# Kernel tuning notes

Hardware: AMD Instinct MI355X
Metric: run time of the kernel (lower is better)

Reference implementation:

```python
import jax, jax.numpy as jnp
import numpy as np

PED = 1024
R_DIM = 128
M_DIM = 128


def setup_inputs() -> dict:
    key = jax.random.key(0)
    k1, k2, k3, k4, k5 = jax.random.split(key, 5)
    hidden_state = jax.random.normal(k1, (PED, M_DIM), dtype=jnp.float32)
    rela_state = jax.random.normal(k2, (PED, PED, R_DIM), dtype=jnp.float32)
    corr_index = jax.random.normal(k3, (PED, PED, 2), dtype=jnp.float32)
    nei_index = jax.random.randint(k4, (PED, PED), 0, 2, dtype=jnp.int32)
    att_w = jax.random.normal(k5, (R_DIM,), dtype=jnp.float32) * 0.2  # nn.Linear weight, std=0.2 init
    att_b = jnp.zeros((1,), dtype=jnp.float32)
    return {"hidden_state": hidden_state, "rela_state": rela_state,
            "corr_index": corr_index, "nei_index": nei_index,
            "att_w": att_w, "att_b": att_b}


def reference(hidden_state, rela_state, corr_index, nei_index, att_w, att_b):
    # hidden_state: [P, M], rela_state: [P, P, R], nei_index: [P, P]
    P = hidden_state.shape[0]
    mask = nei_index.reshape(P, P) > 0                      # [P, P]
    # Linear attention score per (i, j) relation feature
    scores = jnp.einsum('ijr,r->ij', rela_state.reshape(P, P, -1), att_w) + att_b[0]
    # Non-neighbor slots stay 0 then are replaced by -1e-6 (original: Pos[Pos==0] = -1e-6)
    pos = jnp.where(mask, scores, jnp.float32(-1e-6))
    pos = jax.nn.softmax(pos, axis=1)                       # softmax over neighbors j
    # H[i, j] = hidden_state[j] * pos[i, j] where masked, else 0; then sum over j
    weights = jnp.where(mask, pos, 0.0)                     # [P, P]
    H_sum = jnp.einsum('ij,jm->im', weights, hidden_state)  # [P, M]
    return H_sum
```

## Files before the change

kernel.cpp:

```cpp
#include <hip/hip_runtime.h>
#include <math.h>

#define P_DIM 1024
#define R_DIM 128
#define M_DIM 128

__global__ __launch_bounds__(256) void scores_kernel(
    const float* __restrict__ rela,
    const float* __restrict__ att_w,
    const float* __restrict__ att_b,
    float* __restrict__ scores)
{
    const int t    = blockIdx.x * 256 + threadIdx.x;
    const int pair = t >> 5;
    const int lane = t & 31;

    const float4 w4 = reinterpret_cast<const float4*>(att_w)[lane];
    const float4 v  = reinterpret_cast<const float4*>(rela)[(size_t)pair * 32 + lane];

    float s = v.x * w4.x + v.y * w4.y + v.z * w4.z + v.w * w4.w;
    s += __shfl_xor(s, 16);
    s += __shfl_xor(s, 8);
    s += __shfl_xor(s, 4);
    s += __shfl_xor(s, 2);
    s += __shfl_xor(s, 1);

    if (lane == 0) scores[pair] = s + att_b[0];
}

__device__ __forceinline__ float fcomp(const float4& v, int k) {
    return k == 0 ? v.x : k == 1 ? v.y : k == 2 ? v.z : v.w;
}

__global__ __launch_bounds__(256) void attn_kernel(
    const float* __restrict__ scores,
    const int* __restrict__ nei,
    const float* __restrict__ hidden,
    float* __restrict__ out)
{
    __shared__ float  wsm[4][P_DIM];
    __shared__ float4 part[4][8][32];

    const int t    = threadIdx.x;
    const int wid  = t >> 6;
    const int lane = t & 63;
    const int i0   = blockIdx.x << 2;
    const int i    = i0 + wid;

    const float4* s4p = reinterpret_cast<const float4*>(scores + (size_t)i * P_DIM);
    const int4*   n4p = reinterpret_cast<const int4*>(nei + (size_t)i * P_DIM);

    float pv[16];
    unsigned mbits = 0;
    float lmax = -3.0e38f;
    #pragma unroll
    for (int c = 0; c < 4; ++c) {
        const int idx = c * 64 + lane;
        const float4 s4 = s4p[idx];
        const int4   n4 = n4p[idx];
        const float v0 = (n4.x > 0) ? s4.x : -1e-6f;
        const float v1 = (n4.y > 0) ? s4.y : -1e-6f;
        const float v2 = (n4.z > 0) ? s4.z : -1e-6f;
        const float v3 = (n4.w > 0) ? s4.w : -1e-6f;
        mbits |= ((n4.x > 0) ? 1u : 0u) << (c * 4 + 0);
        mbits |= ((n4.y > 0) ? 1u : 0u) << (c * 4 + 1);
        mbits |= ((n4.z > 0) ? 1u : 0u) << (c * 4 + 2);
        mbits |= ((n4.w > 0) ? 1u : 0u) << (c * 4 + 3);
        pv[c * 4 + 0] = v0; pv[c * 4 + 1] = v1;
        pv[c * 4 + 2] = v2; pv[c * 4 + 3] = v3;
        lmax = fmaxf(lmax, fmaxf(fmaxf(v0, v1), fmaxf(v2, v3)));
    }
    #pragma unroll
    for (int off = 32; off >= 1; off >>= 1)
        lmax = fmaxf(lmax, __shfl_xor(lmax, off));

    float lsum = 0.f;
    #pragma unroll
    for (int k = 0; k < 16; ++k) {
        const float e = __expf(pv[k] - lmax);
        pv[k] = e;
        lsum += e;
    }
    #pragma unroll
    for (int off = 32; off >= 1; off >>= 1)
        lsum += __shfl_xor(lsum, off);
    const float inv = 1.0f / lsum;

    #pragma unroll
    for (int c = 0; c < 4; ++c) {
        const int idx = c * 64 + lane;
        float4 o;
        o.x = ((mbits >> (c * 4 + 0)) & 1u) ? pv[c * 4 + 0] * inv : 0.f;
        o.y = ((mbits >> (c * 4 + 1)) & 1u) ? pv[c * 4 + 1] * inv : 0.f;
        o.z = ((mbits >> (c * 4 + 2)) & 1u) ? pv[c * 4 + 2] * inv : 0.f;
        o.w = ((mbits >> (c * 4 + 3)) & 1u) ? pv[c * 4 + 3] * inv : 0.f;
        reinterpret_cast<float4*>(wsm[wid])[idx] = o;
    }
    __syncthreads();

    const int c4 = t & 31;
    const int h  = t >> 5;

    float4 acc[4];
    #pragma unroll
    for (int r = 0; r < 4; ++r) acc[r] = make_float4(0.f, 0.f, 0.f, 0.f);

    const int jbase = h * 128;
    #pragma unroll 2
    for (int jq = 0; jq < 32; ++jq) {
        const int j = jbase + jq * 4;
        float4 wq[4];
        #pragma unroll
        for (int r = 0; r < 4; ++r)
            wq[r] = *reinterpret_cast<const float4*>(&wsm[r][j]);
        float4 hv[4];
        #pragma unroll
        for (int k = 0; k < 4; ++k)
            hv[k] = reinterpret_cast<const float4*>(hidden + (size_t)(j + k) * M_DIM)[c4];
        #pragma unroll
        for (int r = 0; r < 4; ++r) {
            #pragma unroll
            for (int k = 0; k < 4; ++k) {
                const float wc = fcomp(wq[r], k);
                acc[r].x += wc * hv[k].x;
                acc[r].y += wc * hv[k].y;
                acc[r].z += wc * hv[k].z;
                acc[r].w += wc * hv[k].w;
            }
        }
    }

    #pragma unroll
    for (int r = 0; r < 4; ++r) part[r][h][c4] = acc[r];
    __syncthreads();

    if (t < 128) {
        const int r = t >> 5;
        const int c = t & 31;
        float4 sum = part[r][0][c];
        #pragma unroll
        for (int hh = 1; hh < 8; ++hh) {
            const float4 p = part[r][hh][c];
            sum.x += p.x; sum.y += p.y; sum.z += p.z; sum.w += p.w;
        }
        reinterpret_cast<float4*>(out + (size_t)(i0 + r) * M_DIM)[c] = sum;
    }
}

extern "C" void kernel_launch(void* const* d_in, const int* in_sizes, int n_in,
                              void* d_out, int out_size, void* d_ws, size_t ws_size,
                              hipStream_t stream) {
    const float* hidden = (const float*)d_in[0];
    const float* rela   = (const float*)d_in[1];
    const int*   nei    = (const int*)d_in[3];
    const float* att_w  = (const float*)d_in[4];
    const float* att_b  = (const float*)d_in[5];
    float* out    = (float*)d_out;
    float* scores = (float*)d_ws;

    scores_kernel<<<(P_DIM * P_DIM) / 8, 256, 0, stream>>>(rela, att_w, att_b, scores);
    attn_kernel<<<P_DIM / 4, 256, 0, stream>>>(scores, nei, hidden, out);
}
```

Measured before the change: 685.3 us.

## Fuse score computation, softmax and weighted sum into one per-row kernel

Replaces the two-kernel pipeline with a single kernel where each block handles one row i: it computes the relation scores into shared memory, does a block-wide masked softmax, then accumulates the weighted sum of hidden rows. This removes the scores round-trip through global memory and one launch. In exchange the grid shrinks to one block per row, reducing memory-level parallelism on the large rela stream. Each block also rereads all of hidden instead of sharing it across four rows.

```diff
diff --git a/kernel.cpp b/kernel.cpp
--- a/kernel.cpp
+++ b/kernel.cpp
@@ -5,145 +5,104 @@
 #define R_DIM 128
 #define M_DIM 128
 
-__global__ __launch_bounds__(256) void scores_kernel(
+__global__ __launch_bounds__(256) void fused_kernel(
     const float* __restrict__ rela,
+    const int*   __restrict__ nei,
+    const float* __restrict__ hidden,
     const float* __restrict__ att_w,
     const float* __restrict__ att_b,
-    float* __restrict__ scores)
-{
-    const int t    = blockIdx.x * 256 + threadIdx.x;
-    const int pair = t >> 5;
-    const int lane = t & 31;
-
-    const float4 w4 = reinterpret_cast<const float4*>(att_w)[lane];
-    const float4 v  = reinterpret_cast<const float4*>(rela)[(size_t)pair * 32 + lane];
-
-    float s = v.x * w4.x + v.y * w4.y + v.z * w4.z + v.w * w4.w;
-    s += __shfl_xor(s, 16);
-    s += __shfl_xor(s, 8);
-    s += __shfl_xor(s, 4);
-    s += __shfl_xor(s, 2);
-    s += __shfl_xor(s, 1);
-
-    if (lane == 0) scores[pair] = s + att_b[0];
-}
-
-__device__ __forceinline__ float fcomp(const float4& v, int k) {
-    return k == 0 ? v.x : k == 1 ? v.y : k == 2 ? v.z : v.w;
-}
-
-__global__ __launch_bounds__(256) void attn_kernel(
-    const float* __restrict__ scores,
-    const int* __restrict__ nei,
-    const float* __restrict__ hidden,
     float* __restrict__ out)
 {
-    __shared__ float  wsm[4][P_DIM];
-    __shared__ float4 part[4][8][32];
+    __shared__ float  s_lds[P_DIM];
+    __shared__ float  red[8];
+    __shared__ float2 part[4][64];
 
-    const int t    = threadIdx.x;
-    const int wid  = t >> 6;
-    const int lane = t & 63;
-    const int i0   = blockIdx.x << 2;
-    const int i    = i0 + wid;
+    const int t   = threadIdx.x;
+    const int i   = blockIdx.x;
+    const int g   = t >> 5;
+    const int l32 = t & 31;
 
-    const float4* s4p = reinterpret_cast<const float4*>(scores + (size_t)i * P_DIM);
-    const int4*   n4p = reinterpret_cast<const int4*>(nei + (size_t)i * P_DIM);
+    const float4 w4 = reinterpret_cast<const float4*>(att_w)[l32];
+    const float4* rrow =
+        reinterpret_cast<const float4*>(rela + (size_t)i * (P_DIM * R_DIM));
 
-    float pv[16];
-    unsigned mbits = 0;
-    float lmax = -3.0e38f;
-    #pragma unroll
-    for (int c = 0; c < 4; ++c) {
-        const int idx = c * 64 + lane;
-        const float4 s4 = s4p[idx];
-        const int4   n4 = n4p[idx];
-        const float v0 = (n4.x > 0) ? s4.x : -1e-6f;
-        const float v1 = (n4.y > 0) ? s4.y : -1e-6f;
-        const float v2 = (n4.z > 0) ? s4.z : -1e-6f;
-        const float v3 = (n4.w > 0) ? s4.w : -1e-6f;
-        mbits |= ((n4.x > 0) ? 1u : 0u) << (c * 4 + 0);
-        mbits |= ((n4.y > 0) ? 1u : 0u) << (c * 4 + 1);
-        mbits |= ((n4.z > 0) ? 1u : 0u) << (c * 4 + 2);
-        mbits |= ((n4.w > 0) ? 1u : 0u) << (c * 4 + 3);
-        pv[c * 4 + 0] = v0; pv[c * 4 + 1] = v1;
-        pv[c * 4 + 2] = v2; pv[c * 4 + 3] = v3;
-        lmax = fmaxf(lmax, fmaxf(fmaxf(v0, v1), fmaxf(v2, v3)));
+    #pragma unroll 4
+    for (int jq = 0; jq < 128; ++jq) {
+        const int j = jq * 8 + g;
+        const float4 v = rrow[(size_t)j * 32 + l32];
+        float s = v.x * w4.x + v.y * w4.y + v.z * w4.z + v.w * w4.w;
+        s += __shfl_xor(s, 16);
+        s += __shfl_xor(s, 8);
+        s += __shfl_xor(s, 4);
+        s += __shfl_xor(s, 2);
+        s += __shfl_xor(s, 1);
+        if (l32 == 0) s_lds[j] = s;
     }
+    __syncthreads();
+
+    const float bias = att_b[0];
+    const int4  n4 = reinterpret_cast<const int4*>(nei + (size_t)i * P_DIM)[t];
+    const float4 sv = reinterpret_cast<const float4*>(s_lds)[t];
+
+    float v0 = (n4.x > 0) ? sv.x + bias : -1e-6f;
+    float v1 = (n4.y > 0) ? sv.y + bias : -1e-6f;
+    float v2 = (n4.z > 0) ? sv.z + bias : -1e-6f;
+    float v3 = (n4.w > 0) ? sv.w + bias : -1e-6f;
+
+    float lmax = fmaxf(fmaxf(v0, v1), fmaxf(v2, v3));
     #pragma unroll
     for (int off = 32; off >= 1; off >>= 1)
         lmax = fmaxf(lmax, __shfl_xor(lmax, off));
+    if ((t & 63) == 0) red[t >> 6] = lmax;
+    __syncthreads();
+    const float gmax = fmaxf(fmaxf(red[0], red[1]), fmaxf(red[2], red[3]));
 
-    float lsum = 0.f;
-    #pragma unroll
-    for (int k = 0; k < 16; ++k) {
-        const float e = __expf(pv[k] - lmax);
-        pv[k] = e;
-        lsum += e;
-    }
+    const float e0 = __expf(v0 - gmax);
+    const float e1 = __expf(v1 - gmax);
+    const float e2 = __expf(v2 - gmax);
+    const float e3 = __expf(v3 - gmax);
+    float lsum = (e0 + e1) + (e2 + e3);
     #pragma unroll
     for (int off = 32; off >= 1; off >>= 1)
         lsum += __shfl_xor(lsum, off);
-    const float inv = 1.0f / lsum;
+    if ((t & 63) == 0) red[4 + (t >> 6)] = lsum;
+    __syncthreads();
+    const float inv = 1.0f / (red[4] + red[5] + red[6] + red[7]);
 
-    #pragma unroll
-    for (int c = 0; c < 4; ++c) {
-        const int idx = c * 64 + lane;
-        float4 o;
-        o.x = ((mbits >> (c * 4 + 0)) & 1u) ? pv[c * 4 + 0] * inv : 0.f;
-        o.y = ((mbits >> (c * 4 + 1)) & 1u) ? pv[c * 4 + 1] * inv : 0.f;
-        o.z = ((mbits >> (c * 4 + 2)) & 1u) ? pv[c * 4 + 2] * inv : 0.f;
-        o.w = ((mbits >> (c * 4 + 3)) & 1u) ? pv[c * 4 + 3] * inv : 0.f;
-        reinterpret_cast<float4*>(wsm[wid])[idx] = o;
-    }
+    float4 wv;
+    wv.x = (n4.x > 0) ? e0 * inv : 0.f;
+    wv.y = (n4.y > 0) ? e1 * inv : 0.f;
+    wv.z = (n4.z > 0) ? e2 * inv : 0.f;
+    wv.w = (n4.w > 0) ? e3 * inv : 0.f;
+    __syncthreads();
+    reinterpret_cast<float4*>(s_lds)[t] = wv;
     __syncthreads();
 
-    const int c4 = t & 31;
-    const int h  = t >> 5;
+    const int c2 = t & 63;
+    const int q  = t >> 6;
+    const float2* h2 = reinterpret_cast<const float2*>(hidden);
 
-    float4 acc[4];
-    #pragma unroll
-    for (int r = 0; r < 4; ++r) acc[r] = make_float4(0.f, 0.f, 0.f, 0.f);
-
-    const int jbase = h * 128;
-    #pragma unroll 2
-    for (int jq = 0; jq < 32; ++jq) {
-        const int j = jbase + jq * 4;
-        float4 wq[4];
-        #pragma unroll
-        for (int r = 0; r < 4; ++r)
-            wq[r] = *reinterpret_cast<const float4*>(&wsm[r][j]);
-        float4 hv[4];
-        #pragma unroll
-        for (int k = 0; k < 4; ++k)
-            hv[k] = reinterpret_cast<const float4*>(hidden + (size_t)(j + k) * M_DIM)[c4];
-        #pragma unroll
-        for (int r = 0; r < 4; ++r) {
-            #pragma unroll
-            for (int k = 0; k < 4; ++k) {
-                const float wc = fcomp(wq[r], k);
-                acc[r].x += wc * hv[k].x;
-                acc[r].y += wc * hv[k].y;
-                acc[r].z += wc * hv[k].z;
-                acc[r].w += wc * hv[k].w;
-            }
-        }
+    float2 acc = make_float2(0.f, 0.f);
+    const int jb = q * 256;
+    #pragma unroll 4
+    for (int jj = 0; jj < 256; ++jj) {
+        const int j = jb + jj;
+        const float wj = s_lds[j];
+        const float2 h = h2[(size_t)j * 64 + c2];
+        acc.x += wj * h.x;
+        acc.y += wj * h.y;
     }
-
-    #pragma unroll
-    for (int r = 0; r < 4; ++r) part[r][h][c4] = acc[r];
+    part[q][c2] = acc;
     __syncthreads();
 
-    if (t < 128) {
-        const int r = t >> 5;
-        const int c = t & 31;
-        float4 sum = part[r][0][c];
+    if (t < 64) {
+        float2 s = part[0][t];
         #pragma unroll
-        for (int hh = 1; hh < 8; ++hh) {
-            const float4 p = part[r][hh][c];
-            sum.x += p.x; sum.y += p.y; sum.z += p.z; sum.w += p.w;
+        for (int qq = 1; qq < 4; ++qq) {
+            s.x += part[qq][t].x;
+            s.y += part[qq][t].y;
         }
-        reinterpret_cast<float4*>(out + (size_t)(i0 + r) * M_DIM)[c] = sum;
+        reinterpret_cast<float2*>(out + (size_t)i * M_DIM)[t] = s;
     }
 }
 
@@ -155,9 +114,7 @@
     const int*   nei    = (const int*)d_in[3];
     const float* att_w  = (const float*)d_in[4];
     const float* att_b  = (const float*)d_in[5];
-    float* out    = (float*)d_out;
-    float* scores = (float*)d_ws;
+    float* out = (float*)d_out;
 
-    scores_kernel<<<(P_DIM * P_DIM) / 8, 256, 0, stream>>>(rela, att_w, att_b, scores);
-    attn_kernel<<<P_DIM / 4, 256, 0, stream>>>(scores, nei, hidden, out);
+    fused_kernel<<<P_DIM, 256, 0, stream>>>(rela, nei, hidden, att_w, att_b, out);
 }
```

After: 722.5 us. 1.05x slower.

## Skip loading relation rows for non-neighbor pairs in score kernel

Applied to the files above, without the earlier changes.

The score kernel now reads the neighbor mask and only loads the 512-byte relation vector for pairs where the mask is set, writing -1e-6 otherwise. Each wavefront handles 64 pairs, with each half-wave looping over 32 pairs and shuffle-reducing per pair. With a random 0/1 mask this is meant to roughly halve the dominant HBM traffic. The cost is a branchy per-pair loop with many shuffles per wave, and fewer loads in flight per thread than the old fully parallel layout.

```diff
diff --git a/kernel.cpp b/kernel.cpp
--- a/kernel.cpp
+++ b/kernel.cpp
@@ -7,25 +7,46 @@
 
 __global__ __launch_bounds__(256) void scores_kernel(
     const float* __restrict__ rela,
+    const int*   __restrict__ nei,
     const float* __restrict__ att_w,
     const float* __restrict__ att_b,
     float* __restrict__ scores)
 {
-    const int t    = blockIdx.x * 256 + threadIdx.x;
-    const int pair = t >> 5;
-    const int lane = t & 31;
+    const int t    = threadIdx.x;
+    const int wv   = t >> 6;
+    const int lane = t & 63;
+    const int half = lane >> 5;
+    const int l32  = lane & 31;
 
-    const float4 w4 = reinterpret_cast<const float4*>(att_w)[lane];
-    const float4 v  = reinterpret_cast<const float4*>(rela)[(size_t)pair * 32 + lane];
+    const float4 w4   = reinterpret_cast<const float4*>(att_w)[l32];
+    const float  bias = att_b[0];
+    const float4* r4  = reinterpret_cast<const float4*>(rela);
 
-    float s = v.x * w4.x + v.y * w4.y + v.z * w4.z + v.w * w4.w;
-    s += __shfl_xor(s, 16);
-    s += __shfl_xor(s, 8);
-    s += __shfl_xor(s, 4);
-    s += __shfl_xor(s, 2);
-    s += __shfl_xor(s, 1);
+    const int W     = blockIdx.x * 4 + wv;
+    const int pbase = W * 64;
 
-    if (lane == 0) scores[pair] = s + att_b[0];
+    const int n_all = nei[pbase + lane];
+
+    float my_score = -1e-6f;
+
+    #pragma unroll 8
+    for (int it = 0; it < 32; ++it) {
+        const int n = __shfl(n_all, it + 32 * half);
+        const int pair = pbase + 32 * half + it;
+        float s = 0.f;
+        if (n > 0) {
+            const float4 v = r4[(size_t)pair * 32 + l32];
+            s = v.x * w4.x + v.y * w4.y + v.z * w4.z + v.w * w4.w;
+        }
+        s += __shfl_xor(s, 16);
+        s += __shfl_xor(s, 8);
+        s += __shfl_xor(s, 4);
+        s += __shfl_xor(s, 2);
+        s += __shfl_xor(s, 1);
+        if (l32 == it && n > 0) my_score = s + bias;
+    }
+
+    scores[pbase + lane] = my_score;
 }
 
 __device__ __forceinline__ float fcomp(const float4& v, int k) {
@@ -158,6 +179,6 @@
     float* out    = (float*)d_out;
     float* scores = (float*)d_ws;
 
-    scores_kernel<<<(P_DIM * P_DIM) / 8, 256, 0, stream>>>(rela, att_w, att_b, scores);
+    scores_kernel<<<4096, 256, 0, stream>>>(rela, nei, att_w, att_b, scores);
     attn_kernel<<<P_DIM / 4, 256, 0, stream>>>(scores, nei, hidden, out);
 }
```

New measurement: 659.7 us. -3.7%, faster.
